# Kernel optimization log

Measured on AMD Instinct MI355X. Metric: run time of the kernel, lower is better.

The kernel has to match this reference:

```python
import jax, jax.numpy as jnp
from jax import lax
import numpy as np

N, T, V = 32, 32, 128
C_FEAT, C_BOX, C_CLS = 256, 4, 4
C_IN = C_FEAT + C_BOX + C_CLS  # 264 (is_scene=False concatenates x,b,c)
C_OUT = 64
K = 9
EPS = 1e-3  # keras BatchNormalization default epsilon


def _bn4(x, g, b, m, v):
    # inference-mode BN over channel axis 1 of (N,C,T,V)
    s = (g * lax.rsqrt(v + EPS))[None, :, None, None]
    return (x - m[None, :, None, None]) * s + b[None, :, None, None]


def _stgcn(x, a, imp, w, bw, ga, ba, ma, va, al, wt, bt, gb, bb, mb, vb, residual):
    res = x if residual else 0.0
    # SGCN: 1x1 conv (channels_first) then adjacency aggregation; dropout is identity at inference
    h = jnp.einsum('nctv,co->notv', x, w) + bw[None, :, None, None]
    h = jnp.einsum('nctv,ntvw->nctw', h, a * imp)
    # TGCN: BN -> PReLU(alpha per (C,T,V)) -> temporal conv (K,1) SAME -> BN -> (dropout=id)
    h = _bn4(h, ga, ba, ma, va)
    h = jnp.where(h >= 0, h, al[None] * h)
    h = lax.conv_general_dilated(h, wt, (1, 1), 'SAME',
                                 dimension_numbers=('NCHW', 'HWIO', 'NCHW')) + bt[None, :, None, None]
    h = _bn4(h, gb, bb, mb, vb)
    return h + res  # use_mdn=True -> no final PReLU


def _forward(x, b, c, a, dbn_g, dbn_b, dbn_m, dbn_v,
             w0, bw0, imp0, g0a, b0a, m0a, v0a, al0, wt0, bt0, g0b, b0b, m0b, v0b,
             w1, bw1, imp1, g1a, b1a, m1a, v1a, al1, wt1, bt1, g1b, b1b, m1b, v1b):
    x = jnp.concatenate([x, b, c], axis=-1)  # (N,T,V,C_IN)
    n, t, v, cc = x.shape
    # data BN over flattened (V*C) channel axis, exactly as the TF reshapes do
    x = jnp.transpose(x, (0, 2, 3, 1)).reshape(n, v * cc, t)
    s = (dbn_g * lax.rsqrt(dbn_v + EPS))[None, :, None]
    x = (x - dbn_m[None, :, None]) * s + dbn_b[None, :, None]
    # NOTE: the original does transpose(0,1,3,2) then a *reshape* to (N,C,T,V); replicate exactly
    x = x.reshape(n, v, cc, t).transpose(0, 1, 3, 2).reshape(n, cc, t, v)
    x = _stgcn(x, a, imp0, w0, bw0, g0a, b0a, m0a, v0a, al0, wt0, bt0, g0b, b0b, m0b, v0b, residual=False)
    x = _stgcn(x, a, imp1, w1, bw1, g1a, b1a, m1a, v1a, al1, wt1, bt1, g1b, b1b, m1b, v1b, residual=True)
    x = x[:, :, :, 0]  # (N,C_OUT,T)
    return jnp.transpose(x, (0, 2, 1))  # (N,T,C_OUT)


def setup_inputs():
    key = jax.random.key(0)
    ks = jax.random.split(key, 40)
    rn = lambda k, s, sc=1.0: jax.random.normal(k, s, jnp.float32) * sc
    ru = lambda k, s, lo, hi: jax.random.uniform(k, s, jnp.float32, lo, hi)
    d = {}
    d['x'] = rn(ks[0], (N, T, V, C_FEAT))
    d['b'] = rn(ks[1], (N, T, V, C_BOX))
    d['c'] = ru(ks[2], (N, T, V, C_CLS), 0.0, 1.0)
    d['a'] = ru(ks[3], (N, T, V, V), 0.0, 1.0)
    d['dbn_g'] = ru(ks[4], (V * C_IN,), 0.5, 1.5)
    d['dbn_b'] = rn(ks[5], (V * C_IN,), 0.1)
    d['dbn_m'] = rn(ks[6], (V * C_IN,), 0.1)
    d['dbn_v'] = ru(ks[7], (V * C_IN,), 0.5, 1.5)

    def mk_layer(i, cin, kb):
        d['w%d' % i] = rn(ks[kb], (cin, C_OUT), (1.0 / cin) ** 0.5)
        d['bw%d' % i] = rn(ks[kb + 1], (C_OUT,), 0.01)
        d['imp%d' % i] = rn(ks[kb + 2], (V, V), (2.0 / (V * V)) ** 0.5)
        d['g%da' % i] = ru(ks[kb + 3], (C_OUT,), 0.5, 1.5)
        d['b%da' % i] = rn(ks[kb + 4], (C_OUT,), 0.1)
        d['m%da' % i] = rn(ks[kb + 5], (C_OUT,), 0.1)
        d['v%da' % i] = ru(ks[kb + 6], (C_OUT,), 0.5, 1.5)
        d['al%d' % i] = ru(ks[kb + 7], (C_OUT, T, V), 0.0, 0.3)
        d['wt%d' % i] = rn(ks[kb + 8], (K, 1, C_OUT, C_OUT), (1.0 / (K * C_OUT)) ** 0.5)
        d['bt%d' % i] = rn(ks[kb + 9], (C_OUT,), 0.01)
        d['g%db' % i] = ru(ks[kb + 10], (C_OUT,), 0.5, 1.5)
        d['b%db' % i] = rn(ks[kb + 11], (C_OUT,), 0.1)
        d['m%db' % i] = rn(ks[kb + 12], (C_OUT,), 0.1)
        d['v%db' % i] = ru(ks[kb + 13], (C_OUT,), 0.5, 1.5)

    mk_layer(0, C_IN, 8)
    mk_layer(1, C_OUT, 22)
    return d


def reference(x, b, c, a, dbn_g, dbn_b, dbn_m, dbn_v,
              w0, bw0, imp0, g0a, b0a, m0a, v0a, al0, wt0, bt0, g0b, b0b, m0b, v0b,
              w1, bw1, imp1, g1a, b1a, m1a, v1a, al1, wt1, bt1, g1b, b1b, m1b, v1b):
    return _forward(x, b, c, a, dbn_g, dbn_b, dbn_m, dbn_v,
                    w0, bw0, imp0, g0a, b0a, m0a, v0a, al0, wt0, bt0, g0b, b0b, m0b, v0b,
                    w1, bw1, imp1, g1a, b1a, m1a, v1a, al1, wt1, bt1, g1b, b1b, m1b, v1b)
```

## Files before the change

kernel.cpp:

```cpp
#include <hip/hip_runtime.h>
#include <hip/hip_bf16.h>

typedef unsigned short u16;
typedef unsigned int   u32;

#define N_   32
#define T_   32
#define V_   128
#define CIN_ 264
#define CO_  64
#define KT_  9
#define EPS_ 1e-3f

#define OFF_DBN_S 0
#define OFF_DBN_O 33792
#define OFF_W0    67584
#define OFF_BW0   84480
#define OFF_A0S   84544
#define OFF_A0O   84608
#define OFF_B0S   84672
#define OFF_B0O   84736
#define OFF_W1    84800
#define OFF_BW1   88896
#define OFF_A1S   88960
#define OFF_A1O   89024
#define OFF_B1S   89088
#define OFF_B1O   89152
#define PREP_TOTAL 110464

#define B_P    0
#define B_FLAG 360448
#define B_W0A  360512
#define B_WTA  397440
#define B_H0   524288
#define B_XP   (B_H0 + 16777216)
#define B_G0   (B_H0 + 16777216)
#define B_L0   (B_G0 + 16777216)
#define B_G1P  (B_L0 + 33554432)
#define B_END  (B_G1P + 262144)

typedef short bf16x8 __attribute__((ext_vector_type(8)));
typedef float f32x4  __attribute__((ext_vector_type(4)));

__device__ __forceinline__ float bf2f(u16 u) { return __uint_as_float(((u32)u) << 16); }
__device__ __forceinline__ u16 f2bf(float f) {
    u32 x = __float_as_uint(f);
    return (u16)((x + 0x7fffu + ((x >> 16) & 1u)) >> 16);
}
__device__ __forceinline__ float ldin(const void* p, u32 i, int f32) {
    return f32 ? ((const float*)p)[i] : bf2f(((const u16*)p)[i]);
}

__global__ void k_detect(const void* a, int* flag) {
    if (threadIdx.x == 0 && blockIdx.x == 0) {
        const u16* p = (const u16*)a;
        int cnt = 0;
        for (int i = 0; i < 64; ++i) {
            float v = bf2f(p[2 * i]);
            if (v >= 0.f && v <= 1.0f) ++cnt;
        }
        *flag = (cnt >= 56) ? 0 : 1;
    }
}

__global__ void k_prep(const void* dbn_g, const void* dbn_b, const void* dbn_m, const void* dbn_v,
                       const void* w0, const void* bw0,
                       const void* g0a, const void* b0a, const void* m0a, const void* v0a,
                       const void* bt0, const void* g0b, const void* b0b, const void* m0b, const void* v0b,
                       const void* w1, const void* bw1,
                       const void* g1a, const void* b1a, const void* m1a, const void* v1a,
                       const void* bt1, const void* g1b, const void* b1b, const void* m1b, const void* v1b,
                       const void* wt0,
                       float* P, u16* W0A, u16* WTA, const int* flagp)
{
    const int f32 = *flagp;
    int i = blockIdx.x * 256 + threadIdx.x;
    if (i < 33792) {
        float s = ldin(dbn_g, i, f32) * rsqrtf(ldin(dbn_v, i, f32) + EPS_);
        P[OFF_DBN_S + i] = s;
        P[OFF_DBN_O + i] = ldin(dbn_b, i, f32) - ldin(dbn_m, i, f32) * s;
    } else if (i < 50688) { int j = i - 33792; P[OFF_W0 + j] = ldin(w0, j, f32); }
    else if (i < 50752) { int j = i - 50688; P[OFF_BW0 + j] = ldin(bw0, j, f32); }
    else if (i < 50816) { int j = i - 50752;
        float s = ldin(g0a, j, f32) * rsqrtf(ldin(v0a, j, f32) + EPS_);
        P[OFF_A0S + j] = s; P[OFF_A0O + j] = ldin(b0a, j, f32) - ldin(m0a, j, f32) * s;
    } else if (i < 50880) { int j = i - 50816;
        float s = ldin(g0b, j, f32) * rsqrtf(ldin(v0b, j, f32) + EPS_);
        P[OFF_B0S + j] = s; P[OFF_B0O + j] = (ldin(bt0, j, f32) - ldin(m0b, j, f32)) * s + ldin(b0b, j, f32);
    } else if (i < 54976) { int j = i - 50880; P[OFF_W1 + j] = ldin(w1, j, f32); }
    else if (i < 55040) { int j = i - 54976; P[OFF_BW1 + j] = ldin(bw1, j, f32); }
    else if (i < 55104) { int j = i - 55040;
        float s = ldin(g1a, j, f32) * rsqrtf(ldin(v1a, j, f32) + EPS_);
        P[OFF_A1S + j] = s; P[OFF_A1O + j] = ldin(b1a, j, f32) - ldin(m1a, j, f32) * s;
    } else if (i < 55168) { int j = i - 55104;
        float s = ldin(g1b, j, f32) * rsqrtf(ldin(v1b, j, f32) + EPS_);
        P[OFF_B1S + j] = s; P[OFF_B1O + j] = (ldin(bt1, j, f32) - ldin(m1b, j, f32)) * s + ldin(b1b, j, f32);
    } else if (i < 73600) {
        int j = i - 55168; int c = j / 288, ci = j - c * 288;
        float val = (ci < 264) ? ldin(w0, (u32)ci * 64 + c, f32)
                  : ((ci == 264) ? ldin(bw0, c, f32) : 0.f);
        W0A[j] = f2bf(val);
    } else if (i < 110464) {
        int j = i - 73600; int k = j >> 12, rem = j & 4095, o = rem >> 6, ii = rem & 63;
        WTA[j] = f2bf(ldin(wt0, ((u32)(k * 64 + ii)) * 64 + o, f32));
    }
}

__global__ __launch_bounds__(256) void k_bnx(const void* __restrict__ xin, const void* __restrict__ bin,
                                             const void* __restrict__ cin2, const float* __restrict__ P,
                                             u16* __restrict__ Xp, const int* __restrict__ flagp, int nbase)
{
    __shared__ __align__(16) u16 tile[32 * 130];
    const int f32 = *flagp;
    const int rt = blockIdx.x;
    const int ct = blockIdx.y;
    const int nloc = blockIdx.z;
    const int n = nbase + nloc;
    const int c0 = ct * 32;
    const int ncols = (ct == 8) ? 8 : 32;
    const int r0 = rt * 128;
    const int tid = threadIdx.x;

    for (int q = tid; q < ncols * 32; q += 256) {
        int j = q >> 5, i4 = (q & 31) << 2;
        u32 L = (u32)(c0 + j) * 4096u + (u32)(r0 + i4);
        u32 vs = L / 8448u;
        u32 r  = L - vs * 8448u;
        u32 ts = r / 264u;
        u32 cc = r - ts * 264u;
        u32 base = ((u32)n * 32u + ts) * 128u + vs;
        float4 val;
        if (f32) {
            if (cc < 256u)      val = *(const float4*)((const float*)xin  + (size_t)base * 256u + cc);
            else if (cc < 260u) val = *(const float4*)((const float*)bin  + (size_t)base * 4u + (cc - 256u));
            else                val = *(const float4*)((const float*)cin2 + (size_t)base * 4u + (cc - 260u));
        } else {
            ushort4 uv;
            if (cc < 256u)      uv = *(const ushort4*)((const u16*)xin  + (size_t)base * 256u + cc);
            else if (cc < 260u) uv = *(const ushort4*)((const u16*)bin  + (size_t)base * 4u + (cc - 256u));
            else                uv = *(const ushort4*)((const u16*)cin2 + (size_t)base * 4u + (cc - 260u));
            val.x = bf2f(uv.x); val.y = bf2f(uv.y); val.z = bf2f(uv.z); val.w = bf2f(uv.w);
        }
        u32 ch = vs * 264u + cc;
        const float4 s4 = *(const float4*)&P[OFF_DBN_S + ch];
        const float4 o4 = *(const float4*)&P[OFF_DBN_O + ch];
        ushort2 lo, hi;
        lo.x = f2bf(fmaf(val.x, s4.x, o4.x));
        lo.y = f2bf(fmaf(val.y, s4.y, o4.y));
        hi.x = f2bf(fmaf(val.z, s4.z, o4.z));
        hi.y = f2bf(fmaf(val.w, s4.w, o4.w));
        *(ushort2*)&tile[j * 130 + i4]     = lo;
        *(ushort2*)&tile[j * 130 + i4 + 2] = hi;
    }
    __syncthreads();
    const int chunks = ncols >> 3;
    for (int e = tid; e < 128 * chunks; e += 256) {
        int i, cch;
        if (chunks == 4) { i = e >> 2; cch = e & 3; } else { i = e; cch = 0; }
        __align__(16) u16 tmp[8];
#pragma unroll
        for (int k2 = 0; k2 < 8; ++k2) tmp[k2] = tile[(cch * 8 + k2) * 130 + i];
        *(uint4*)&Xp[((u32)nloc * 4096u + (u32)(r0 + i)) * 264u + (u32)(c0 + cch * 8)] = *(uint4*)tmp;
    }
}

__global__ __launch_bounds__(256) void k_pw0(const u16* __restrict__ Xp, const u16* __restrict__ W0Ag,
                                             u16* __restrict__ h0, int nbase)
{
    const int t2 = blockIdx.x, nloc = blockIdx.y, vh = blockIdx.z;
    const int n = nbase + nloc;
    const int tid = threadIdx.x;
    const int wv = tid >> 6, lane = tid & 63, l16 = lane & 15, quad = lane >> 4;
    const int m0 = wv * 16;
    const int vrow = vh * 64 + m0 + l16;
    const u16* arow = Xp + ((u32)nloc * 4096u + (u32)(t2 * 128 + vrow)) * 264u;

    f32x4 acc[4];
#pragma unroll
    for (int i = 0; i < 4; ++i) acc[i] = (f32x4){0.f, 0.f, 0.f, 0.f};

#pragma unroll
    for (int ks = 0; ks < 8; ++ks) {
        const int k0 = ks * 32 + quad * 8;
        bf16x8 af = *(const bf16x8*)&arow[k0];
#pragma unroll
        for (int ni = 0; ni < 4; ++ni) {
            bf16x8 bf = *(const bf16x8*)&W0Ag[(u32)(ni * 16 + l16) * 288 + k0];
            acc[ni] = __builtin_amdgcn_mfma_f32_16x16x32_bf16(af, bf, acc[ni], 0, 0, 0);
        }
    }
    {
        bf16x8 af = (bf16x8){0, 0, 0, 0, 0, 0, 0, 0};
        if (quad == 0)      af = *(const bf16x8*)&arow[256];
        else if (quad == 1) af[0] = (short)0x3F80;
        const int k0 = 256 + quad * 8;
#pragma unroll
        for (int ni = 0; ni < 4; ++ni) {
            bf16x8 bf = *(const bf16x8*)&W0Ag[(u32)(ni * 16 + l16) * 288 + k0];
            acc[ni] = __builtin_amdgcn_mfma_f32_16x16x32_bf16(af, bf, acc[ni], 0, 0, 0);
        }
    }
    const int v = vh * 64 + m0 + quad * 4;
#pragma unroll
    for (int ni = 0; ni < 4; ++ni) {
        int c = ni * 16 + l16;
        ushort4 rr; u16* rp = (u16*)&rr;
#pragma unroll
        for (int r = 0; r < 4; ++r) rp[r] = f2bf(acc[ni][r]);
        *(ushort4*)&h0[((u32)(n * 64 + c) * 32 + t2) * 128 + v] = rr;
    }
}

__global__ __launch_bounds__(256) void k_at(const void* __restrict__ a, const void* __restrict__ imp0,
                                            u16* __restrict__ aT, const int* __restrict__ flagp)
{
    __shared__ __align__(16) u16 tile[128 * 128];
    const int f32 = *flagp;
    const int t = blockIdx.x, n = blockIdx.y;
    const int tid = threadIdx.x;
    const u32 abase = (((u32)n * 32u + (u32)t) * 128u) * 128u;

    for (int e = tid; e < 2048; e += 256) {
        int v = e >> 4, w0 = (e & 15) << 3;
        float vals[8];
        if (f32) {
            const float* ap = (const float*)a + abase + (u32)v * 128u + w0;
            const float* ip = (const float*)imp0 + (u32)v * 128u + w0;
            float4 x0 = *(const float4*)ap, x1 = *(const float4*)(ap + 4);
            float4 i0 = *(const float4*)ip, i1 = *(const float4*)(ip + 4);
            vals[0] = x0.x * i0.x; vals[1] = x0.y * i0.y; vals[2] = x0.z * i0.z; vals[3] = x0.w * i0.w;
            vals[4] = x1.x * i1.x; vals[5] = x1.y * i1.y; vals[6] = x1.z * i1.z; vals[7] = x1.w * i1.w;
        } else {
            uint4 xu = *(const uint4*)((const u16*)a + abase + (u32)v * 128u + w0);
            uint4 iu = *(const uint4*)((const u16*)imp0 + (u32)v * 128u + w0);
            const u16* xp = (const u16*)&xu; const u16* ip = (const u16*)&iu;
#pragma unroll
            for (int j = 0; j < 8; ++j) vals[j] = bf2f(xp[j]) * bf2f(ip[j]);
        }
        __align__(16) u16 pk[8];
#pragma unroll
        for (int j = 0; j < 8; ++j) pk[j] = f2bf(vals[j]);
        u32 byte = (u32)v * 256u + (((u32)w0 * 2u) ^ ((((u32)v >> 3) & 7u) << 4));
        *(uint4*)((char*)tile + byte) = *(uint4*)pk;
    }
    __syncthreads();
    for (int e = tid; e < 2048; e += 256) {
        int w = e >> 4, v0 = (e & 15) << 3;
        __align__(16) u16 tmp[8];
#pragma unroll
        for (int k = 0; k < 8; ++k) {
            int v = v0 + k;
            u32 byte = (u32)v * 256u + ((((u32)w * 2u)) ^ ((((u32)v >> 3) & 7u) << 4));
            tmp[k] = *(const u16*)((const char*)tile + byte);
        }
        *(uint4*)&aT[abase + (u32)w * 128u + v0] = *(uint4*)tmp;
    }
}

__global__ __launch_bounds__(256) void k_graph0(const void* __restrict__ al0, const float* __restrict__ P,
                                                const u16* __restrict__ h0, const u16* __restrict__ aT,
                                                u16* __restrict__ g0, const int* __restrict__ flagp)
{
    const int f32 = *flagp;
    const int t = blockIdx.x, n = blockIdx.y;
    const int tid = threadIdx.x;
    const int wv = tid >> 6, lane = tid & 63, l16 = lane & 15, quad = lane >> 4;
    const int n0w = wv * 32;
    const u16* aTb = aT + (((u32)n * 32u + (u32)t) * 128u) * 128u;
    const u16* Hb  = h0 + ((u32)n * 2048u + (u32)t) * 128u;

    f32x4 acc[4][2];
#pragma unroll
    for (int mi = 0; mi < 4; ++mi) { acc[mi][0] = (f32x4){0,0,0,0}; acc[mi][1] = (f32x4){0,0,0,0}; }
#pragma unroll
    for (int ks = 0; ks < 4; ++ks) {
        const int k0 = ks * 32 + quad * 8;
        bf16x8 bf0 = *(const bf16x8*)&aTb[(u32)(n0w + l16) * 128u + k0];
        bf16x8 bf1 = *(const bf16x8*)&aTb[(u32)(n0w + 16 + l16) * 128u + k0];
#pragma unroll
        for (int mi = 0; mi < 4; ++mi) {
            bf16x8 af = *(const bf16x8*)&Hb[(u32)(mi * 16 + l16) * 4096u + k0];
            acc[mi][0] = __builtin_amdgcn_mfma_f32_16x16x32_bf16(af, bf0, acc[mi][0], 0, 0, 0);
            acc[mi][1] = __builtin_amdgcn_mfma_f32_16x16x32_bf16(af, bf1, acc[mi][1], 0, 0, 0);
        }
    }
#pragma unroll
    for (int mi = 0; mi < 4; ++mi) {
        const int c0 = mi * 16 + quad * 4;
        const float4 s4 = *(const float4*)&P[OFF_A0S + c0];
        const float4 o4 = *(const float4*)&P[OFF_A0O + c0];
        const float ss[4] = {s4.x, s4.y, s4.z, s4.w};
        const float oo[4] = {o4.x, o4.y, o4.z, o4.w};
#pragma unroll
        for (int ni = 0; ni < 2; ++ni) {
            const int w = n0w + ni * 16 + l16;
            ushort4 rr; u16* rp = (u16*)&rr;
#pragma unroll
            for (int r = 0; r < 4; ++r) {
                float y = fmaf(acc[mi][ni][r], ss[r], oo[r]);
                float alv = ldin(al0, ((u32)(c0 + r) * 32 + t) * 128 + w, f32);
                rp[r] = f2bf((y >= 0.f) ? y : alv * y);
            }
            *(ushort4*)&g0[((u32)(n * 32 + t) * 128 + w) * 64 + c0] = rr;
        }
    }
}

__global__ __launch_bounds__(256) void k_tconv0(const u16* __restrict__ WTAg, const float* __restrict__ P,
                                                const u16* __restrict__ g0, float* __restrict__ L0)
{
    const int t = blockIdx.x, n = blockIdx.y;
    const int tid = threadIdx.x;
    const int kmin = (t < 4) ? (4 - t) : 0;
    const int kmax = (t > 27) ? (35 - t) : 8;
    const int wv = tid >> 6, lane = tid & 63, l16 = lane & 15, quad = lane >> 4;
    const int n0w = wv * 32;

    f32x4 acc[4][2];
#pragma unroll
    for (int mi = 0; mi < 4; ++mi) { acc[mi][0] = (f32x4){0,0,0,0}; acc[mi][1] = (f32x4){0,0,0,0}; }

    for (int k = kmin; k <= kmax; ++k) {
        const u16* Wb = WTAg + (u32)k * 4096u;
        const u16* Bb = g0 + ((u32)(n * 32 + (t + k - 4)) * 128u) * 64u;
#pragma unroll
        for (int ks = 0; ks < 2; ++ks) {
            const int k0 = ks * 32 + quad * 8;
            bf16x8 bf0 = *(const bf16x8*)&Bb[(u32)(n0w + l16) * 64u + k0];
            bf16x8 bf1 = *(const bf16x8*)&Bb[(u32)(n0w + 16 + l16) * 64u + k0];
#pragma unroll
            for (int mi = 0; mi < 4; ++mi) {
                bf16x8 af = *(const bf16x8*)&Wb[(u32)(mi * 16 + l16) * 64u + k0];
                acc[mi][0] = __builtin_amdgcn_mfma_f32_16x16x32_bf16(af, bf0, acc[mi][0], 0, 0, 0);
                acc[mi][1] = __builtin_amdgcn_mfma_f32_16x16x32_bf16(af, bf1, acc[mi][1], 0, 0, 0);
            }
        }
    }
#pragma unroll
    for (int mi = 0; mi < 4; ++mi) {
        const int ob = mi * 16 + quad * 4;
        const float4 s4 = *(const float4*)&P[OFF_B0S + ob];
        const float4 o4 = *(const float4*)&P[OFF_B0O + ob];
        const float ss[4] = {s4.x, s4.y, s4.z, s4.w};
        const float oo[4] = {o4.x, o4.y, o4.z, o4.w};
#pragma unroll
        for (int ni = 0; ni < 2; ++ni) {
            const int v = n0w + ni * 16 + l16;
#pragma unroll
            for (int r = 0; r < 4; ++r)
                L0[((u32)(n * 64 + ob + r) * 32 + t) * 128 + v] = fmaf(acc[mi][ni][r], ss[r], oo[r]);
        }
    }
}

__global__ __launch_bounds__(256) void k_pw1(const void* __restrict__ a, const void* __restrict__ imp1,
                                             const void* __restrict__ al1, const float* __restrict__ P,
                                             const float* __restrict__ L0, float* __restrict__ g1p,
                                             const int* __restrict__ flagp)
{
    __shared__ float amv[V_];
    __shared__ float xr[CO_];
    __shared__ float Ssh;
    const int f32 = *flagp;
    const int t = blockIdx.x, n = blockIdx.y;
    const int tid = threadIdx.x;

    if (tid < V_) {
        float av = ldin(a, (((u32)n * T_ + t) * V_ + tid) * V_ + 0u, f32)
                 * ldin(imp1, (u32)tid * V_ + 0u, f32);
        amv[tid] = av;
    }
    __syncthreads();
    if (tid < 64) {
        float s = amv[tid] + amv[tid + 64];
#pragma unroll
        for (int m = 1; m < 64; m <<= 1) s += __shfl_xor(s, m);
        if (tid == 0) Ssh = s;
    }
    const int c = tid >> 2, sub = tid & 3;
    const float* Lrow = L0 + (u32)n * (CO_ * T_ * V_) + (u32)c * (T_ * V_) + (u32)t * V_ + sub * 32;
    float p = 0.f;
#pragma unroll
    for (int j = 0; j < 32; j += 4) {
        float4 x = *(const float4*)(Lrow + j);
        float4 m = *(const float4*)&amv[sub * 32 + j];
        p = fmaf(x.x, m.x, p); p = fmaf(x.y, m.y, p);
        p = fmaf(x.z, m.z, p); p = fmaf(x.w, m.w, p);
    }
    p += __shfl_xor(p, 1);
    p += __shfl_xor(p, 2);
    if (sub == 0) xr[c] = p;
    __syncthreads();
    if (tid < CO_) {
        const int o = tid;
        float y = P[OFF_BW1 + o] * Ssh;
        for (int cc = 0; cc < CO_; ++cc)
            y = fmaf(xr[cc], P[OFF_W1 + cc * CO_ + o], y);
        y = fmaf(y, P[OFF_A1S + o], P[OFF_A1O + o]);
        float alv = ldin(al1, ((u32)o * T_ + t) * V_ + 0u, f32);
        y = (y >= 0.f) ? y : alv * y;
        g1p[((u32)n * CO_ + o) * T_ + t] = y;
    }
}

__global__ __launch_bounds__(64) void k_tconv1(const void* __restrict__ wt1, const float* __restrict__ P,
                                               const float* __restrict__ g1p, const float* __restrict__ L0,
                                               void* __restrict__ out, const int* __restrict__ flagp)
{
    __shared__ float gl[CO_ * KT_];
    const int f32 = *flagp;
    const int t = blockIdx.x, n = blockIdx.y;
    const int tid = threadIdx.x;
    for (int e = tid; e < CO_ * KT_; e += 64) {
        int i = e / KT_, kk = e - i * KT_;
        int tt = t + kk - 4;
        gl[e] = (tt >= 0 && tt < T_) ? g1p[((u32)n * CO_ + i) * T_ + tt] : 0.f;
    }
    __syncthreads();
    float acc = 0.f;
    for (int i = 0; i < CO_; ++i) {
#pragma unroll
        for (int k = 0; k < KT_; ++k) {
            float wv = ldin(wt1, ((u32)(k * CO_ + i)) * CO_ + tid, f32);
            acc = fmaf(gl[i * KT_ + k], wv, acc);
        }
    }
    float y = fmaf(acc, P[OFF_B1S + tid], P[OFF_B1O + tid]);
    y += L0[(u32)n * (CO_ * T_ * V_) + (u32)tid * (T_ * V_) + (u32)t * V_ + 0];
    const u32 oi = ((u32)n * T_ + t) * CO_ + tid;
    if (f32) ((float*)out)[oi] = y;
    else     ((u16*)out)[oi]   = f2bf(y);
}

__global__ void k_fail(u16* out, int nel) {
    int i = blockIdx.x * 256 + threadIdx.x;
    if (i < nel) out[i] = 0x7f80;
}

extern "C" void kernel_launch(void* const* d_in, const int* in_sizes, int n_in,
                              void* d_out, int out_size, void* d_ws, size_t ws_size,
                              hipStream_t stream)
{
    const void* xin  = d_in[0];
    const void* bin  = d_in[1];
    const void* cin2 = d_in[2];
    const void* a    = d_in[3];
    const void* dbn_g = d_in[4];
    const void* dbn_b = d_in[5];
    const void* dbn_m = d_in[6];
    const void* dbn_v = d_in[7];
    const void* w0  = d_in[8];
    const void* bw0 = d_in[9];
    const void* imp0 = d_in[10];
    const void* g0a = d_in[11];
    const void* b0a = d_in[12];
    const void* m0a = d_in[13];
    const void* v0a = d_in[14];
    const void* al0 = d_in[15];
    const void* wt0 = d_in[16];
    const void* bt0 = d_in[17];
    const void* g0b = d_in[18];
    const void* b0b = d_in[19];
    const void* m0b = d_in[20];
    const void* v0b = d_in[21];
    const void* w1  = d_in[22];
    const void* bw1 = d_in[23];
    const void* imp1 = d_in[24];
    const void* g1a = d_in[25];
    const void* b1a = d_in[26];
    const void* m1a = d_in[27];
    const void* v1a = d_in[28];
    const void* al1 = d_in[29];
    const void* wt1 = d_in[30];
    const void* bt1 = d_in[31];
    const void* g1b = d_in[32];
    const void* b1b = d_in[33];
    const void* m1b = d_in[34];
    const void* v1b = d_in[35];

    if (ws_size < (size_t)B_END) {
        k_fail<<<(out_size + 255) / 256, 256, 0, stream>>>((u16*)d_out, out_size);
        return;
    }
    char* w = (char*)d_ws;
    float* P    = (float*)(w + B_P);
    int*   flg  = (int*)(w + B_FLAG);
    u16*   W0A  = (u16*)(w + B_W0A);
    u16*   WTA  = (u16*)(w + B_WTA);
    u16*   h0   = (u16*)(w + B_H0);
    u16*   Xp   = (u16*)(w + B_XP);
    u16*   g0   = (u16*)(w + B_G0);
    u16*   aT   = (u16*)(w + B_L0);
    float* L0   = (float*)(w + B_L0);
    float* g1p  = (float*)(w + B_G1P);

    k_detect<<<1, 64, 0, stream>>>(a, flg);
    k_prep<<<(PREP_TOTAL + 255) / 256, 256, 0, stream>>>(
        dbn_g, dbn_b, dbn_m, dbn_v, w0, bw0, g0a, b0a, m0a, v0a,
        bt0, g0b, b0b, m0b, v0b, w1, bw1, g1a, b1a, m1a, v1a,
        bt1, g1b, b1b, m1b, v1b, wt0, P, W0A, WTA, flg);

    for (int hf = 0; hf < 2; ++hf) {
        const int nbase = hf * 16;
        k_bnx<<<dim3(32, 9, 16), 256, 0, stream>>>(xin, bin, cin2, P, Xp, flg, nbase);
        k_pw0<<<dim3(T_, 16, 2), 256, 0, stream>>>(Xp, W0A, h0, nbase);
    }

    dim3 grid(T_, N_);
    k_at    <<<grid, 256, 0, stream>>>(a, imp0, aT, flg);
    k_graph0<<<grid, 256, 0, stream>>>(al0, P, h0, aT, g0, flg);
    k_tconv0<<<grid, 256, 0, stream>>>(WTA, P, g0, L0);
    k_pw1   <<<grid, 256, 0, stream>>>(a, imp1, al1, P, L0, g1p, flg);
    k_tconv1<<<grid,  64, 0, stream>>>(wt1, P, g1p, L0, d_out, flg);
}
```

Baseline: 523.0 us.

## Fuse adjacency transpose into graph kernel, unsplit batch halves, retile tconv1

The adjacency transpose kernel is merged into the graph-aggregation kernel, which now builds the transposed adjacency tile in swizzled shared memory and reads B fragments directly from it. This removes a global write and read of the transposed matrix. The two-half batch loop for the input BN and first pointwise GEMM is collapsed into single full-batch launches, using a larger separate workspace buffer. The final temporal conv now uses one 256-thread block per sample, with each thread computing 8 time steps from a shared sliding window so weight loads are reused, in place of one 64-thread block per time step.

```diff
diff --git a/kernel.cpp b/kernel.cpp
--- a/kernel.cpp
+++ b/kernel.cpp
@@ -33,11 +33,11 @@
 #define B_W0A  360512
 #define B_WTA  397440
 #define B_H0   524288
-#define B_XP   (B_H0 + 16777216)
 #define B_G0   (B_H0 + 16777216)
 #define B_L0   (B_G0 + 16777216)
 #define B_G1P  (B_L0 + 33554432)
-#define B_END  (B_G1P + 262144)
+#define B_XP2  (B_G1P + 262144)
+#define B_END  (B_XP2 + 69206016)
 
 typedef short bf16x8 __attribute__((ext_vector_type(8)));
 typedef float f32x4  __attribute__((ext_vector_type(4)));
@@ -49,6 +49,10 @@
 }
 __device__ __forceinline__ float ldin(const void* p, u32 i, int f32) {
     return f32 ? ((const float*)p)[i] : bf2f(((const u16*)p)[i]);
+}
+__device__ __forceinline__ u32 swzv(u32 v) {
+    u32 m = (v >> 3) & 7u;
+    return (m << 4) ^ ((m & 3u) << 5);
 }
 
 __global__ void k_detect(const void* a, int* flag) {
@@ -108,14 +112,13 @@
 
 __global__ __launch_bounds__(256) void k_bnx(const void* __restrict__ xin, const void* __restrict__ bin,
                                              const void* __restrict__ cin2, const float* __restrict__ P,
-                                             u16* __restrict__ Xp, const int* __restrict__ flagp, int nbase)
+                                             u16* __restrict__ Xp, const int* __restrict__ flagp)
 {
     __shared__ __align__(16) u16 tile[32 * 130];
     const int f32 = *flagp;
     const int rt = blockIdx.x;
     const int ct = blockIdx.y;
-    const int nloc = blockIdx.z;
-    const int n = nbase + nloc;
+    const int n  = blockIdx.z;
     const int c0 = ct * 32;
     const int ncols = (ct == 8) ? 8 : 32;
     const int r0 = rt * 128;
@@ -160,20 +163,19 @@
         __align__(16) u16 tmp[8];
 #pragma unroll
         for (int k2 = 0; k2 < 8; ++k2) tmp[k2] = tile[(cch * 8 + k2) * 130 + i];
-        *(uint4*)&Xp[((u32)nloc * 4096u + (u32)(r0 + i)) * 264u + (u32)(c0 + cch * 8)] = *(uint4*)tmp;
+        *(uint4*)&Xp[((u32)n * 4096u + (u32)(r0 + i)) * 264u + (u32)(c0 + cch * 8)] = *(uint4*)tmp;
     }
 }
 
 __global__ __launch_bounds__(256) void k_pw0(const u16* __restrict__ Xp, const u16* __restrict__ W0Ag,
-                                             u16* __restrict__ h0, int nbase)
-{
-    const int t2 = blockIdx.x, nloc = blockIdx.y, vh = blockIdx.z;
-    const int n = nbase + nloc;
+                                             u16* __restrict__ h0)
+{
+    const int t2 = blockIdx.x, n = blockIdx.y, vh = blockIdx.z;
     const int tid = threadIdx.x;
     const int wv = tid >> 6, lane = tid & 63, l16 = lane & 15, quad = lane >> 4;
     const int m0 = wv * 16;
     const int vrow = vh * 64 + m0 + l16;
-    const u16* arow = Xp + ((u32)nloc * 4096u + (u32)(t2 * 128 + vrow)) * 264u;
+    const u16* arow = Xp + ((u32)n * 4096u + (u32)(t2 * 128 + vrow)) * 264u;
 
     f32x4 acc[4];
 #pragma unroll
@@ -211,8 +213,10 @@
     }
 }
 
-__global__ __launch_bounds__(256) void k_at(const void* __restrict__ a, const void* __restrict__ imp0,
-                                            u16* __restrict__ aT, const int* __restrict__ flagp)
+__global__ __launch_bounds__(256) void k_graph0(const void* __restrict__ a, const void* __restrict__ imp0,
+                                                const void* __restrict__ al0, const float* __restrict__ P,
+                                                const u16* __restrict__ h0, u16* __restrict__ g0,
+                                                const int* __restrict__ flagp)
 {
     __shared__ __align__(16) u16 tile[128 * 128];
     const int f32 = *flagp;
@@ -240,34 +244,14 @@
         __align__(16) u16 pk[8];
 #pragma unroll
         for (int j = 0; j < 8; ++j) pk[j] = f2bf(vals[j]);
-        u32 byte = (u32)v * 256u + (((u32)w0 * 2u) ^ ((((u32)v >> 3) & 7u) << 4));
+        u32 byte = (u32)v * 256u + (((u32)w0 * 2u) ^ swzv((u32)v));
         *(uint4*)((char*)tile + byte) = *(uint4*)pk;
     }
     __syncthreads();
-    for (int e = tid; e < 2048; e += 256) {
-        int w = e >> 4, v0 = (e & 15) << 3;
-        __align__(16) u16 tmp[8];
-#pragma unroll
-        for (int k = 0; k < 8; ++k) {
-            int v = v0 + k;
-            u32 byte = (u32)v * 256u + ((((u32)w * 2u)) ^ ((((u32)v >> 3) & 7u) << 4));
-            tmp[k] = *(const u16*)((const char*)tile + byte);
-        }
-        *(uint4*)&aT[abase + (u32)w * 128u + v0] = *(uint4*)tmp;
-    }
-}
-
-__global__ __launch_bounds__(256) void k_graph0(const void* __restrict__ al0, const float* __restrict__ P,
-                                                const u16* __restrict__ h0, const u16* __restrict__ aT,
-                                                u16* __restrict__ g0, const int* __restrict__ flagp)
-{
-    const int f32 = *flagp;
-    const int t = blockIdx.x, n = blockIdx.y;
-    const int tid = threadIdx.x;
+
     const int wv = tid >> 6, lane = tid & 63, l16 = lane & 15, quad = lane >> 4;
     const int n0w = wv * 32;
-    const u16* aTb = aT + (((u32)n * 32u + (u32)t) * 128u) * 128u;
-    const u16* Hb  = h0 + ((u32)n * 2048u + (u32)t) * 128u;
+    const u16* Hb = h0 + ((u32)n * 2048u + (u32)t) * 128u;
 
     f32x4 acc[4][2];
 #pragma unroll
@@ -275,8 +259,16 @@
 #pragma unroll
     for (int ks = 0; ks < 4; ++ks) {
         const int k0 = ks * 32 + quad * 8;
-        bf16x8 bf0 = *(const bf16x8*)&aTb[(u32)(n0w + l16) * 128u + k0];
-        bf16x8 bf1 = *(const bf16x8*)&aTb[(u32)(n0w + 16 + l16) * 128u + k0];
+        const u32 xr = swzv((u32)k0);
+        const u32 wb0 = (u32)(n0w + l16) * 2u;
+        const u32 wb1 = (u32)(n0w + 16 + l16) * 2u;
+        bf16x8 bf0, bf1;
+#pragma unroll
+        for (int j = 0; j < 8; ++j) {
+            const u32 rb = (u32)(k0 + j) * 256u;
+            bf0[j] = (short)*(const u16*)((const char*)tile + rb + (wb0 ^ xr));
+            bf1[j] = (short)*(const u16*)((const char*)tile + rb + (wb1 ^ xr));
+        }
 #pragma unroll
         for (int mi = 0; mi < 4; ++mi) {
             bf16x8 af = *(const bf16x8*)&Hb[(u32)(mi * 16 + l16) * 4096u + k0];
@@ -403,33 +395,48 @@
     }
 }
 
-__global__ __launch_bounds__(64) void k_tconv1(const void* __restrict__ wt1, const float* __restrict__ P,
-                                               const float* __restrict__ g1p, const float* __restrict__ L0,
-                                               void* __restrict__ out, const int* __restrict__ flagp)
-{
-    __shared__ float gl[CO_ * KT_];
+__global__ __launch_bounds__(256) void k_tconv1(const void* __restrict__ wt1, const float* __restrict__ P,
+                                                const float* __restrict__ g1p, const float* __restrict__ L0,
+                                                void* __restrict__ out, const int* __restrict__ flagp)
+{
+    __shared__ float gl[CO_][40];
     const int f32 = *flagp;
-    const int t = blockIdx.x, n = blockIdx.y;
+    const int n = blockIdx.x;
     const int tid = threadIdx.x;
-    for (int e = tid; e < CO_ * KT_; e += 64) {
-        int i = e / KT_, kk = e - i * KT_;
-        int tt = t + kk - 4;
-        gl[e] = (tt >= 0 && tt < T_) ? g1p[((u32)n * CO_ + i) * T_ + tt] : 0.f;
+    for (int e = tid; e < 512; e += 256) {
+        int i = e >> 3, p = e & 7;
+        gl[i][(p < 4) ? p : (p + 32)] = 0.f;
+    }
+    for (int e = tid; e < 2048; e += 256) {
+        int i = e >> 5, tt = e & 31;
+        gl[i][tt + 4] = g1p[(u32)n * 2048u + (u32)i * 32u + tt];
     }
     __syncthreads();
-    float acc = 0.f;
+    const int o = tid & 63, tq = tid >> 6, t0 = tq * 8;
+    float acc[8];
+#pragma unroll
+    for (int j = 0; j < 8; ++j) acc[j] = 0.f;
     for (int i = 0; i < CO_; ++i) {
+        float win[16];
+#pragma unroll
+        for (int m = 0; m < 16; m += 4) *(float4*)&win[m] = *(const float4*)&gl[i][t0 + m];
 #pragma unroll
         for (int k = 0; k < KT_; ++k) {
-            float wv = ldin(wt1, ((u32)(k * CO_ + i)) * CO_ + tid, f32);
-            acc = fmaf(gl[i * KT_ + k], wv, acc);
-        }
-    }
-    float y = fmaf(acc, P[OFF_B1S + tid], P[OFF_B1O + tid]);
-    y += L0[(u32)n * (CO_ * T_ * V_) + (u32)tid * (T_ * V_) + (u32)t * V_ + 0];
-    const u32 oi = ((u32)n * T_ + t) * CO_ + tid;
-    if (f32) ((float*)out)[oi] = y;
-    else     ((u16*)out)[oi]   = f2bf(y);
+            float wv = ldin(wt1, ((u32)(k * CO_ + i)) * CO_ + o, f32);
+#pragma unroll
+            for (int j = 0; j < 8; ++j) acc[j] = fmaf(win[j + k], wv, acc[j]);
+        }
+    }
+    const float s1 = P[OFF_B1S + o], o1 = P[OFF_B1O + o];
+#pragma unroll
+    for (int j = 0; j < 8; ++j) {
+        const int t = t0 + j;
+        float y = fmaf(acc[j], s1, o1);
+        y += L0[(u32)n * (CO_ * T_ * V_) + (u32)o * (T_ * V_) + (u32)t * V_ + 0];
+        const u32 oi = ((u32)n * T_ + t) * CO_ + o;
+        if (f32) ((float*)out)[oi] = y;
+        else     ((u16*)out)[oi]   = f2bf(y);
+    }
 }
 
 __global__ void k_fail(u16* out, int nel) {
@@ -488,11 +495,10 @@
     u16*   W0A  = (u16*)(w + B_W0A);
     u16*   WTA  = (u16*)(w + B_WTA);
     u16*   h0   = (u16*)(w + B_H0);
-    u16*   Xp   = (u16*)(w + B_XP);
     u16*   g0   = (u16*)(w + B_G0);
-    u16*   aT   = (u16*)(w + B_L0);
     float* L0   = (float*)(w + B_L0);
     float* g1p  = (float*)(w + B_G1P);
+    u16*   Xp   = (u16*)(w + B_XP2);
 
     k_detect<<<1, 64, 0, stream>>>(a, flg);
     k_prep<<<(PREP_TOTAL + 255) / 256, 256, 0, stream>>>(
@@ -500,16 +506,11 @@
         bt0, g0b, b0b, m0b, v0b, w1, bw1, g1a, b1a, m1a, v1a,
         bt1, g1b, b1b, m1b, v1b, wt0, P, W0A, WTA, flg);
 
-    for (int hf = 0; hf < 2; ++hf) {
-        const int nbase = hf * 16;
-        k_bnx<<<dim3(32, 9, 16), 256, 0, stream>>>(xin, bin, cin2, P, Xp, flg, nbase);
-        k_pw0<<<dim3(T_, 16, 2), 256, 0, stream>>>(Xp, W0A, h0, nbase);
-    }
-
     dim3 grid(T_, N_);
-    k_at    <<<grid, 256, 0, stream>>>(a, imp0, aT, flg);
-    k_graph0<<<grid, 256, 0, stream>>>(al0, P, h0, aT, g0, flg);
+    k_bnx   <<<dim3(32, 9, 32), 256, 0, stream>>>(xin, bin, cin2, P, Xp, flg);
+    k_pw0   <<<dim3(T_, N_, 2), 256, 0, stream>>>(Xp, W0A, h0);
+    k_graph0<<<grid, 256, 0, stream>>>(a, imp0, al0, P, h0, g0, flg);
     k_tconv0<<<grid, 256, 0, stream>>>(WTA, P, g0, L0);
     k_pw1   <<<grid, 256, 0, stream>>>(a, imp1, al1, P, L0, g1p, flg);
-    k_tconv1<<<grid,  64, 0, stream>>>(wt1, P, g1p, L0, d_out, flg);
-}
+    k_tconv1<<<dim3(N_), 256, 0, stream>>>(wt1, P, g1p, L0, d_out, flg);
+}
```

New measurement: 506.5 us. 3.2% less time.
